# Performance work log

Measured on AMD Instinct MI355X. Metric: run time of the kernel, lower is better.

Reference implementation:

```python
import jax, jax.numpy as jnp
import numpy as np

D_MODEL = 1024
N_HEADS = 16
HEAD_DIM = D_MODEL // N_HEADS  # 64
N_T = max(1, int(N_HEADS * 0.25))  # 4 time heads
N_S = N_HEADS - N_T               # 12 space heads
T_DIM = N_T * HEAD_DIM
S_DIM = N_S * HEAD_DIM
B, L = 2, 2048


def setup_inputs() -> dict:
    key = jax.random.key(0)
    ks = jax.random.split(key, 8)
    std = 0.02
    return {
        "x": jax.random.normal(ks[0], (B, L, D_MODEL), dtype=jnp.float32),
        "attention_mask": jnp.zeros((B, 1, 1, L), dtype=jnp.float32),
        # torch nn.Linear weights have shape (out_features, in_features)
        "w_qt": jax.random.normal(ks[1], (T_DIM, D_MODEL), dtype=jnp.float32) * std,
        "w_kt": jax.random.normal(ks[2], (T_DIM, D_MODEL), dtype=jnp.float32) * std,
        "w_qs": jax.random.normal(ks[3], (S_DIM, D_MODEL), dtype=jnp.float32) * std,
        "w_ks": jax.random.normal(ks[4], (S_DIM, D_MODEL), dtype=jnp.float32) * std,
        "w_sigma": jnp.zeros((1,), dtype=jnp.float32),
        "w_v": jax.random.normal(ks[5], (D_MODEL, D_MODEL), dtype=jnp.float32) * std,
        "w_o": jax.random.normal(ks[6], (D_MODEL, D_MODEL), dtype=jnp.float32) * std,
    }


def _heads(x, w, n_h):
    # x:(B,L,D) @ w.T:(D,out) -> (B,L,n_h,d_h) -> (B,n_h,L,d_h)
    b, l, _ = x.shape
    y = jnp.einsum('bld,td->blt', x, w)
    return y.reshape(b, l, n_h, HEAD_DIM).transpose(0, 2, 1, 3)


def reference(x, attention_mask, w_qt, w_kt, w_qs, w_ks, w_sigma, w_v, w_o):
    b, l, _ = x.shape
    scale = np.sqrt(HEAD_DIM).astype(np.float32)
    # F3: time heads (sign-flipped, scaled by learnable sigma) + space heads
    Qt = _heads(x, w_qt, N_T)
    Kt = _heads(x, w_kt, N_T)
    Qs = _heads(x, w_qs, N_S)
    Ks = _heads(x, w_ks, N_S)
    st = jnp.einsum('bhqd,bhkd->bhqk', Qt, Kt)  # (B,N_T,L,L)
    ss = jnp.einsum('bhqd,bhkd->bhqk', Qs, Ks)  # (B,N_S,L,L)
    sigma = jax.nn.sigmoid(w_sigma[0])
    score = jnp.concatenate([-sigma * st, ss], axis=1) / scale  # (B,H,L,L)
    score = score + attention_mask.astype(score.dtype)
    attn_probs = jax.nn.softmax(score, axis=-1).astype(x.dtype)
    # dropout p=0.0 -> identity
    V = _heads(x, w_v, N_HEADS)  # (B,H,L,d_h)
    out = jnp.einsum('bhqk,bhkd->bhqd', attn_probs, V)
    out = out.transpose(0, 2, 1, 3).reshape(b, l, D_MODEL)
    out = jnp.einsum('bld,od->blo', out, w_o)
    return out, attn_probs
```

## Files before the change

kernel.cpp:

```cpp
#include <hip/hip_runtime.h>

typedef __bf16 bf16x8 __attribute__((ext_vector_type(8)));
typedef float f32x4 __attribute__((ext_vector_type(4)));
typedef short short4v __attribute__((ext_vector_type(4)));
typedef unsigned short ushort8 __attribute__((ext_vector_type(8)));

#define AS1 __attribute__((address_space(1)))
#define AS3 __attribute__((address_space(3)))
#define GLL16(g, l) __builtin_amdgcn_global_load_lds((const AS1 void*)(g), (AS3 void*)(l), 16, 0, 0)
#define MFMA16(a, b, c) __builtin_amdgcn_mfma_f32_16x16x32_bf16((a), (b), (c), 0, 0, 0)

__device__ __forceinline__ unsigned short f2bf(float f) {
  unsigned int u = __builtin_bit_cast(unsigned int, f);
  u = (u + 0x7fffu + ((u >> 16) & 1u)) >> 16;
  return (unsigned short)u;
}

__global__ void convert_kernel(const float* __restrict__ x,
                               const float* __restrict__ w_qt, const float* __restrict__ w_kt,
                               const float* __restrict__ w_qs, const float* __restrict__ w_ks,
                               const float* __restrict__ w_v, const float* __restrict__ w_o,
                               unsigned short* __restrict__ xb, unsigned short* __restrict__ wcat,
                               unsigned short* __restrict__ wob) {
  const int NX = 4096 * 1024, NW = 3072 * 1024, NO = 1024 * 1024;
  int stride = gridDim.x * blockDim.x;
  for (int i = blockIdx.x * blockDim.x + threadIdx.x; i < NX + NW + NO; i += stride) {
    if (i < NX) {
      xb[i] = f2bf(x[i]);
    } else if (i < NX + NW) {
      int j = i - NX;
      int n = j >> 10, k = j & 1023;
      const float* src;
      if (n < 256)        src = w_qt + n * 1024;
      else if (n < 1024)  src = w_qs + (n - 256) * 1024;
      else if (n < 1280)  src = w_kt + (n - 1024) * 1024;
      else if (n < 2048)  src = w_ks + (n - 1280) * 1024;
      else                src = w_v + (n - 2048) * 1024;
      wcat[j] = f2bf(src[k]);
    } else {
      int j = i - NX - NW;
      wob[j] = f2bf(w_o[j]);
    }
  }
}

__global__ __launch_bounds__(256) void gemm_qkv(const unsigned short* __restrict__ A,
                                                const unsigned short* __restrict__ Bw,
                                                unsigned short* __restrict__ qb,
                                                unsigned short* __restrict__ kb,
                                                unsigned short* __restrict__ vt) {
  __shared__ unsigned short As[128 * 32];
  __shared__ unsigned short Bs[128 * 32];
  const int t = threadIdx.x;
  const int lane = t & 63, wid = t >> 6;
  const int wm = wid >> 1, wn = wid & 1;
  const int lr = lane & 15, lg = lane >> 4;
  const int m0 = blockIdx.x * 128, n0 = blockIdx.y * 128;
  const int K = 1024;
  f32x4 acc[4][4] = {};
  const unsigned short* gA0 = A + (m0 + (t >> 2)) * K + (t & 3) * 8;
  const unsigned short* gB0 = Bw + (n0 + (t >> 2)) * K + (t & 3) * 8;
  char* lA = (char*)As + wid * 1024;
  char* lB = (char*)Bs + wid * 1024;
  for (int k0 = 0; k0 < K; k0 += 32) {
    __syncthreads();
    GLL16(gA0 + k0, lA);
    GLL16(gA0 + 64 * K + k0, lA + 4096);
    GLL16(gB0 + k0, lB);
    GLL16(gB0 + 64 * K + k0, lB + 4096);
    __syncthreads();
    bf16x8 af[4], bfr[4];
#pragma unroll
    for (int i = 0; i < 4; ++i) {
      af[i] = *(const bf16x8*)&As[(wm * 64 + i * 16 + lr) * 32 + lg * 8];
      bfr[i] = *(const bf16x8*)&Bs[(wn * 64 + i * 16 + lr) * 32 + lg * 8];
    }
#pragma unroll
    for (int i = 0; i < 4; ++i)
#pragma unroll
      for (int j = 0; j < 4; ++j)
        acc[i][j] = MFMA16(af[i], bfr[j], acc[i][j]);
  }
#pragma unroll
  for (int i = 0; i < 4; ++i) {
#pragma unroll
    for (int j = 0; j < 4; ++j) {
      int n = n0 + wn * 64 + j * 16 + lr;
      int mb = m0 + wm * 64 + i * 16 + lg * 4;
      f32x4 v = acc[i][j];
      if (n < 2048) {
        unsigned short* dst = (n < 1024) ? qb : kb;
        int nn = n & 1023;
        int h = nn >> 6, d = nn & 63;
#pragma unroll
        for (int r = 0; r < 4; ++r) {
          int m = mb + r;
          int b = m >> 11, l = m & 2047;
          dst[((b * 16 + h) * 2048 + l) * 64 + d] = f2bf(v[r]);
        }
      } else {
        int nn = n - 2048;
        int h = nn >> 6, d = nn & 63;
        int b = mb >> 11, l = mb & 2047;
        short4v pk;
        pk[0] = (short)f2bf(v[0]); pk[1] = (short)f2bf(v[1]);
        pk[2] = (short)f2bf(v[2]); pk[3] = (short)f2bf(v[3]);
        *(short4v*)&vt[((b * 16 + h) * 64 + d) * 2048 + l] = pk;
      }
    }
  }
}

__global__ __launch_bounds__(256, 4) void attn_kernel(const unsigned short* __restrict__ qb,
                                                      const unsigned short* __restrict__ kb,
                                                      const unsigned short* __restrict__ vt,
                                                      const float* __restrict__ mask,
                                                      const float* __restrict__ w_sigma,
                                                      float* __restrict__ probs,
                                                      unsigned short* __restrict__ ao) {
  __shared__ __align__(16) unsigned short ebuf[2][4][1280];
  __shared__ __align__(16) float pvacc[2048];
  __shared__ float psum[4][32];
  __shared__ float rinv[32];
  const int t = threadIdx.x;
  const int lane = t & 63, w = t >> 6;
  const int lr = lane & 15, lg = lane >> 4;
  const int q0 = blockIdx.x * 32;
  const int bh = blockIdx.y;
  const int b = bh >> 4, h = bh & 15;
  const float sigma = 1.0f / (1.0f + __expf(-w_sigma[0]));
  const float fac = (h < 4) ? (-sigma * 0.125f) : 0.125f;
  const float* maskb = mask + b * 2048;
  const int kbase = w * 512;

  for (int i = t; i < 2048; i += 256) pvacc[i] = 0.0f;

  bf16x8 aq[2][2];
#pragma unroll
  for (int qt = 0; qt < 2; ++qt) {
    const unsigned short* qp = qb + ((bh * 2048) + q0 + qt * 16 + lr) * 64 + lg * 8;
    aq[qt][0] = *(const bf16x8*)qp;
    aq[qt][1] = *(const bf16x8*)(qp + 32);
  }

  float rs[2][4] = {};
  for (int c = 0; c < 16; ++c) {
    int kc = kbase + c * 32;
#pragma unroll
    for (int kt = 0; kt < 2; ++kt) {
      int col = kc + kt * 16 + lr;
      const unsigned short* kp = kb + ((bh * 2048) + col) * 64 + lg * 8;
      bf16x8 b0 = *(const bf16x8*)kp;
      bf16x8 b1 = *(const bf16x8*)(kp + 32);
      float mv = maskb[col];
#pragma unroll
      for (int qt = 0; qt < 2; ++qt) {
        f32x4 acc = {};
        acc = MFMA16(aq[qt][0], b0, acc);
        acc = MFMA16(aq[qt][1], b1, acc);
#pragma unroll
        for (int r = 0; r < 4; ++r) rs[qt][r] += __expf(acc[r] * fac + mv);
      }
    }
  }
#pragma unroll
  for (int o = 1; o < 16; o <<= 1)
#pragma unroll
    for (int qt = 0; qt < 2; ++qt)
#pragma unroll
      for (int r = 0; r < 4; ++r) rs[qt][r] += __shfl_xor(rs[qt][r], o);
  if (lr == 0) {
#pragma unroll
    for (int qt = 0; qt < 2; ++qt)
#pragma unroll
      for (int r = 0; r < 4; ++r) psum[w][qt * 16 + lg * 4 + r] = rs[qt][r];
  }
  __syncthreads();
  if (t < 32) rinv[t] = 1.0f / (psum[0][t] + psum[1][t] + psum[2][t] + psum[3][t]);
  __syncthreads();

  float rv[2][4];
#pragma unroll
  for (int qt = 0; qt < 2; ++qt)
#pragma unroll
    for (int r = 0; r < 4; ++r) rv[qt][r] = rinv[qt * 16 + lg * 4 + r];

  float* pp = probs + (long long)(bh * 2048 + q0) * 2048;
  f32x4 pv[2][4] = {};
  for (int c = 0; c < 16; ++c) {
    int kc = kbase + c * 32;
    unsigned short* eb = &ebuf[c & 1][w][0];
#pragma unroll
    for (int kt = 0; kt < 2; ++kt) {
      int col = kc + kt * 16 + lr;
      const unsigned short* kp = kb + ((bh * 2048) + col) * 64 + lg * 8;
      bf16x8 b0 = *(const bf16x8*)kp;
      bf16x8 b1 = *(const bf16x8*)(kp + 32);
      float mv = maskb[col];
#pragma unroll
      for (int qt = 0; qt < 2; ++qt) {
        f32x4 acc = {};
        acc = MFMA16(aq[qt][0], b0, acc);
        acc = MFMA16(aq[qt][1], b1, acc);
#pragma unroll
        for (int r = 0; r < 4; ++r) {
          float ev = __expf(acc[r] * fac + mv);
          eb[(qt * 16 + lg * 4 + r) * 40 + kt * 16 + lr] = f2bf(ev);
          __builtin_nontemporal_store(ev * rv[qt][r],
              &pp[(qt * 16 + lg * 4 + r) * 2048 + kt * 16 + lr + kc]);
        }
      }
    }
    asm volatile("s_waitcnt lgkmcnt(0)" ::: "memory");
    bf16x8 pa[2];
#pragma unroll
    for (int qt = 0; qt < 2; ++qt)
      pa[qt] = *(const bf16x8*)&eb[(qt * 16 + lr) * 40 + lg * 8];
#pragma unroll
    for (int dt = 0; dt < 4; ++dt) {
      const unsigned short* vp = vt + ((bh * 64) + dt * 16 + lr) * 2048 + kc + lg * 8;
      bf16x8 bv = *(const bf16x8*)vp;
      pv[0][dt] = MFMA16(pa[0], bv, pv[0][dt]);
      pv[1][dt] = MFMA16(pa[1], bv, pv[1][dt]);
    }
  }

#pragma unroll
  for (int qt = 0; qt < 2; ++qt)
#pragma unroll
    for (int dt = 0; dt < 4; ++dt)
#pragma unroll
      for (int r = 0; r < 4; ++r)
        atomicAdd(&pvacc[(qt * 16 + lg * 4 + r) * 64 + dt * 16 + lr], pv[qt][dt][r]);
  __syncthreads();

  {
    int row = t >> 3, c8 = (t & 7) * 8;
    f32x4 v0 = *(const f32x4*)&pvacc[row * 64 + c8];
    f32x4 v1 = *(const f32x4*)&pvacc[row * 64 + c8 + 4];
    float ri = rinv[row];
    ushort8 o;
#pragma unroll
    for (int i = 0; i < 4; ++i) {
      o[i] = f2bf(v0[i] * ri);
      o[i + 4] = f2bf(v1[i] * ri);
    }
    *(ushort8*)&ao[((b * 2048) + q0 + row) * 1024 + h * 64 + c8] = o;
  }
}

__global__ __launch_bounds__(256) void gemm_oproj(const unsigned short* __restrict__ A,
                                                  const unsigned short* __restrict__ Bw,
                                                  float* __restrict__ out) {
  __shared__ unsigned short As[128 * 32];
  __shared__ unsigned short Bs[128 * 32];
  const int t = threadIdx.x;
  const int lane = t & 63, wid = t >> 6;
  const int wm = wid >> 1, wn = wid & 1;
  const int lr = lane & 15, lg = lane >> 4;
  const int m0 = blockIdx.x * 128, n0 = blockIdx.y * 128;
  const int K = 1024;
  f32x4 acc[4][4] = {};
  const unsigned short* gA0 = A + (m0 + (t >> 2)) * K + (t & 3) * 8;
  const unsigned short* gB0 = Bw + (n0 + (t >> 2)) * K + (t & 3) * 8;
  char* lA = (char*)As + wid * 1024;
  char* lB = (char*)Bs + wid * 1024;
  for (int k0 = 0; k0 < K; k0 += 32) {
    __syncthreads();
    GLL16(gA0 + k0, lA);
    GLL16(gA0 + 64 * K + k0, lA + 4096);
    GLL16(gB0 + k0, lB);
    GLL16(gB0 + 64 * K + k0, lB + 4096);
    __syncthreads();
    bf16x8 af[4], bfr[4];
#pragma unroll
    for (int i = 0; i < 4; ++i) {
      af[i] = *(const bf16x8*)&As[(wm * 64 + i * 16 + lr) * 32 + lg * 8];
      bfr[i] = *(const bf16x8*)&Bs[(wn * 64 + i * 16 + lr) * 32 + lg * 8];
    }
#pragma unroll
    for (int i = 0; i < 4; ++i)
#pragma unroll
      for (int j = 0; j < 4; ++j)
        acc[i][j] = MFMA16(af[i], bfr[j], acc[i][j]);
  }
#pragma unroll
  for (int i = 0; i < 4; ++i) {
#pragma unroll
    for (int j = 0; j < 4; ++j) {
      int n = n0 + wn * 64 + j * 16 + lr;
      int mb = m0 + wm * 64 + i * 16 + lg * 4;
#pragma unroll
      for (int r = 0; r < 4; ++r)
        out[(mb + r) * 1024 + n] = acc[i][j][r];
    }
  }
}

extern "C" void kernel_launch(void* const* d_in, const int* in_sizes, int n_in,
                              void* d_out, int out_size, void* d_ws, size_t ws_size,
                              hipStream_t stream) {
  const float* x       = (const float*)d_in[0];
  const float* amask   = (const float*)d_in[1];
  const float* w_qt    = (const float*)d_in[2];
  const float* w_kt    = (const float*)d_in[3];
  const float* w_qs    = (const float*)d_in[4];
  const float* w_ks    = (const float*)d_in[5];
  const float* w_sigma = (const float*)d_in[6];
  const float* w_v     = (const float*)d_in[7];
  const float* w_o     = (const float*)d_in[8];

  char* ws = (char*)d_ws;
  unsigned short* xb   = (unsigned short*)ws;
  unsigned short* wcat = (unsigned short*)(ws + 8388608);
  unsigned short* wob  = (unsigned short*)(ws + 14680064);
  unsigned short* qb   = (unsigned short*)(ws + 16777216);
  unsigned short* kb   = (unsigned short*)(ws + 25165824);
  unsigned short* vt   = (unsigned short*)(ws + 33554432);
  unsigned short* ao   = (unsigned short*)(ws + 41943040);

  float* outp = (float*)d_out;
  float* probs = outp + 4194304;

  convert_kernel<<<2048, 256, 0, stream>>>(x, w_qt, w_kt, w_qs, w_ks, w_v, w_o, xb, wcat, wob);
  gemm_qkv<<<dim3(32, 24), 256, 0, stream>>>(xb, wcat, qb, kb, vt);
  attn_kernel<<<dim3(64, 32), 256, 0, stream>>>(qb, kb, vt, amask, w_sigma, probs, ao);
  gemm_oproj<<<dim3(32, 8), 256, 0, stream>>>(ao, wob, outp);
}
```

Baseline: 340.5 us.

## Split attention into row-sum and main kernels with pre-normalized probabilities and vectorized stores

Moves the first softmax pass into a separate kernel that handles 64 query rows per block and writes the per-row negative log2 of the denominator. The main kernel then adds that term inside exp2, so probabilities come out already normalized and the final per-row rescale disappears. The probabilities are staged as fp32 in an XOR-swizzled LDS buffer, written to global memory as vectorized 16-byte nontemporal stores, and packed to bf16 with v_cvt_pk_bf16_f32 for the PV MFMA. This is meant to coalesce the large probs write and reduce exp and convert overhead, at the cost of an extra launch and a second full read of K for QK^T.

```diff
diff --git a/kernel.cpp b/kernel.cpp
--- a/kernel.cpp
+++ b/kernel.cpp
@@ -4,16 +4,24 @@
 typedef float f32x4 __attribute__((ext_vector_type(4)));
 typedef short short4v __attribute__((ext_vector_type(4)));
 typedef unsigned short ushort8 __attribute__((ext_vector_type(8)));
+typedef unsigned int uint4v __attribute__((ext_vector_type(4)));
 
 #define AS1 __attribute__((address_space(1)))
 #define AS3 __attribute__((address_space(3)))
 #define GLL16(g, l) __builtin_amdgcn_global_load_lds((const AS1 void*)(g), (AS3 void*)(l), 16, 0, 0)
 #define MFMA16(a, b, c) __builtin_amdgcn_mfma_f32_16x16x32_bf16((a), (b), (c), 0, 0, 0)
+#define L2E 1.44269504f
 
 __device__ __forceinline__ unsigned short f2bf(float f) {
   unsigned int u = __builtin_bit_cast(unsigned int, f);
   u = (u + 0x7fffu + ((u >> 16) & 1u)) >> 16;
   return (unsigned short)u;
+}
+
+__device__ __forceinline__ unsigned int cvtpk_bf16(float lo, float hi) {
+  unsigned int r;
+  asm("v_cvt_pk_bf16_f32 %0, %1, %2" : "=v"(r) : "v"(lo), "v"(hi));
+  return r;
 }
 
 __global__ void convert_kernel(const float* __restrict__ x,
@@ -111,17 +119,80 @@
   }
 }
 
-__global__ __launch_bounds__(256, 4) void attn_kernel(const unsigned short* __restrict__ qb,
+__global__ __launch_bounds__(256, 4) void attn_rowsum(const unsigned short* __restrict__ qb,
                                                       const unsigned short* __restrict__ kb,
-                                                      const unsigned short* __restrict__ vt,
                                                       const float* __restrict__ mask,
                                                       const float* __restrict__ w_sigma,
-                                                      float* __restrict__ probs,
-                                                      unsigned short* __restrict__ ao) {
-  __shared__ __align__(16) unsigned short ebuf[2][4][1280];
+                                                      float* __restrict__ rws) {
+  __shared__ float psum[4][64];
+  const int t = threadIdx.x;
+  const int lane = t & 63, w = t >> 6;
+  const int lr = lane & 15, lg = lane >> 4;
+  const int q0 = blockIdx.x * 64;
+  const int bh = blockIdx.y;
+  const int b = bh >> 4, h = bh & 15;
+  const float sigma = 1.0f / (1.0f + __expf(-w_sigma[0]));
+  const float fac2 = ((h < 4) ? (-sigma * 0.125f) : 0.125f) * L2E;
+  const float* maskb = mask + b * 2048;
+  const int kbase = w * 512;
+
+  bf16x8 aq[4][2];
+#pragma unroll
+  for (int qt = 0; qt < 4; ++qt) {
+    const unsigned short* qp = qb + ((bh * 2048) + q0 + qt * 16 + lr) * 64 + lg * 8;
+    aq[qt][0] = *(const bf16x8*)qp;
+    aq[qt][1] = *(const bf16x8*)(qp + 32);
+  }
+
+  float rs[4][4] = {};
+  for (int c = 0; c < 16; ++c) {
+    int kc = kbase + c * 32;
+#pragma unroll
+    for (int kt = 0; kt < 2; ++kt) {
+      int col = kc + kt * 16 + lr;
+      const unsigned short* kp = kb + ((bh * 2048) + col) * 64 + lg * 8;
+      bf16x8 b0 = *(const bf16x8*)kp;
+      bf16x8 b1 = *(const bf16x8*)(kp + 32);
+      float mv2 = maskb[col] * L2E;
+#pragma unroll
+      for (int qt = 0; qt < 4; ++qt) {
+        f32x4 acc = {};
+        acc = MFMA16(aq[qt][0], b0, acc);
+        acc = MFMA16(aq[qt][1], b1, acc);
+#pragma unroll
+        for (int r = 0; r < 4; ++r) rs[qt][r] += exp2f(acc[r] * fac2 + mv2);
+      }
+    }
+  }
+#pragma unroll
+  for (int o = 1; o < 16; o <<= 1)
+#pragma unroll
+    for (int qt = 0; qt < 4; ++qt)
+#pragma unroll
+      for (int r = 0; r < 4; ++r) rs[qt][r] += __shfl_xor(rs[qt][r], o);
+  if (lr == 0) {
+#pragma unroll
+    for (int qt = 0; qt < 4; ++qt)
+#pragma unroll
+      for (int r = 0; r < 4; ++r) psum[w][qt * 16 + lg * 4 + r] = rs[qt][r];
+  }
+  __syncthreads();
+  if (t < 64) {
+    float s = psum[0][t] + psum[1][t] + psum[2][t] + psum[3][t];
+    rws[bh * 2048 + q0 + t] = -log2f(s);
+  }
+}
+
+__global__ __launch_bounds__(256, 4) void attn_main(const unsigned short* __restrict__ qb,
+                                                    const unsigned short* __restrict__ kb,
+                                                    const unsigned short* __restrict__ vt,
+                                                    const float* __restrict__ mask,
+                                                    const float* __restrict__ w_sigma,
+                                                    const float* __restrict__ rws,
+                                                    float* __restrict__ probs,
+                                                    unsigned short* __restrict__ ao) {
+  __shared__ __align__(16) char ebuf[4][4096];
   __shared__ __align__(16) float pvacc[2048];
-  __shared__ float psum[4][32];
-  __shared__ float rinv[32];
   const int t = threadIdx.x;
   const int lane = t & 63, w = t >> 6;
   const int lr = lane & 15, lg = lane >> 4;
@@ -129,21 +200,28 @@
   const int bh = blockIdx.y;
   const int b = bh >> 4, h = bh & 15;
   const float sigma = 1.0f / (1.0f + __expf(-w_sigma[0]));
-  const float fac = (h < 4) ? (-sigma * 0.125f) : 0.125f;
+  const float fac2 = ((h < 4) ? (-sigma * 0.125f) : 0.125f) * L2E;
   const float* maskb = mask + b * 2048;
   const int kbase = w * 512;
 
   for (int i = t; i < 2048; i += 256) pvacc[i] = 0.0f;
+  __syncthreads();
 
   bf16x8 aq[2][2];
+  float lr2[2][4];
 #pragma unroll
   for (int qt = 0; qt < 2; ++qt) {
     const unsigned short* qp = qb + ((bh * 2048) + q0 + qt * 16 + lr) * 64 + lg * 8;
     aq[qt][0] = *(const bf16x8*)qp;
     aq[qt][1] = *(const bf16x8*)(qp + 32);
-  }
-
-  float rs[2][4] = {};
+#pragma unroll
+    for (int r = 0; r < 4; ++r)
+      lr2[qt][r] = rws[bh * 2048 + q0 + qt * 16 + lg * 4 + r];
+  }
+
+  char* eb = ebuf[w];
+  float* pp = probs + (long long)(bh * 2048 + q0) * 2048;
+  f32x4 pv[2][4] = {};
   for (int c = 0; c < 16; ++c) {
     int kc = kbase + c * 32;
 #pragma unroll
@@ -152,70 +230,40 @@
       const unsigned short* kp = kb + ((bh * 2048) + col) * 64 + lg * 8;
       bf16x8 b0 = *(const bf16x8*)kp;
       bf16x8 b1 = *(const bf16x8*)(kp + 32);
-      float mv = maskb[col];
+      float mv2 = maskb[col] * L2E;
 #pragma unroll
       for (int qt = 0; qt < 2; ++qt) {
         f32x4 acc = {};
         acc = MFMA16(aq[qt][0], b0, acc);
         acc = MFMA16(aq[qt][1], b1, acc);
 #pragma unroll
-        for (int r = 0; r < 4; ++r) rs[qt][r] += __expf(acc[r] * fac + mv);
-      }
-    }
-  }
-#pragma unroll
-  for (int o = 1; o < 16; o <<= 1)
-#pragma unroll
-    for (int qt = 0; qt < 2; ++qt)
-#pragma unroll
-      for (int r = 0; r < 4; ++r) rs[qt][r] += __shfl_xor(rs[qt][r], o);
-  if (lr == 0) {
-#pragma unroll
-    for (int qt = 0; qt < 2; ++qt)
-#pragma unroll
-      for (int r = 0; r < 4; ++r) psum[w][qt * 16 + lg * 4 + r] = rs[qt][r];
-  }
-  __syncthreads();
-  if (t < 32) rinv[t] = 1.0f / (psum[0][t] + psum[1][t] + psum[2][t] + psum[3][t]);
-  __syncthreads();
-
-  float rv[2][4];
-#pragma unroll
-  for (int qt = 0; qt < 2; ++qt)
-#pragma unroll
-    for (int r = 0; r < 4; ++r) rv[qt][r] = rinv[qt * 16 + lg * 4 + r];
-
-  float* pp = probs + (long long)(bh * 2048 + q0) * 2048;
-  f32x4 pv[2][4] = {};
-  for (int c = 0; c < 16; ++c) {
-    int kc = kbase + c * 32;
-    unsigned short* eb = &ebuf[c & 1][w][0];
-#pragma unroll
-    for (int kt = 0; kt < 2; ++kt) {
-      int col = kc + kt * 16 + lr;
-      const unsigned short* kp = kb + ((bh * 2048) + col) * 64 + lg * 8;
-      bf16x8 b0 = *(const bf16x8*)kp;
-      bf16x8 b1 = *(const bf16x8*)(kp + 32);
-      float mv = maskb[col];
-#pragma unroll
-      for (int qt = 0; qt < 2; ++qt) {
-        f32x4 acc = {};
-        acc = MFMA16(aq[qt][0], b0, acc);
-        acc = MFMA16(aq[qt][1], b1, acc);
-#pragma unroll
         for (int r = 0; r < 4; ++r) {
-          float ev = __expf(acc[r] * fac + mv);
-          eb[(qt * 16 + lg * 4 + r) * 40 + kt * 16 + lr] = f2bf(ev);
-          __builtin_nontemporal_store(ev * rv[qt][r],
-              &pp[(qt * 16 + lg * 4 + r) * 2048 + kt * 16 + lr + kc]);
+          int row = qt * 16 + lg * 4 + r;
+          float p = exp2f(acc[r] * fac2 + mv2 + lr2[qt][r]);
+          int off = (row * 128 + (kt * 16 + lr) * 4) ^ ((row & 7) << 4);
+          *(float*)(eb + off) = p;
         }
       }
     }
     asm volatile("s_waitcnt lgkmcnt(0)" ::: "memory");
     bf16x8 pa[2];
 #pragma unroll
-    for (int qt = 0; qt < 2; ++qt)
-      pa[qt] = *(const bf16x8*)&eb[(qt * 16 + lr) * 40 + lg * 8];
+    for (int qt = 0; qt < 2; ++qt) {
+      int row = qt * 16 + lr;
+      int base = row * 128 + lg * 32;
+      int sw = (row & 7) << 4;
+      f32x4 v0 = *(const f32x4*)(eb + (base ^ sw));
+      f32x4 v1 = *(const f32x4*)(eb + ((base + 16) ^ sw));
+      float* dst = pp + row * 2048 + kc + lg * 8;
+      __builtin_nontemporal_store(v0, (f32x4*)dst);
+      __builtin_nontemporal_store(v1, (f32x4*)(dst + 4));
+      uint4v u;
+      u[0] = cvtpk_bf16(v0[0], v0[1]);
+      u[1] = cvtpk_bf16(v0[2], v0[3]);
+      u[2] = cvtpk_bf16(v1[0], v1[1]);
+      u[3] = cvtpk_bf16(v1[2], v1[3]);
+      pa[qt] = __builtin_bit_cast(bf16x8, u);
+    }
 #pragma unroll
     for (int dt = 0; dt < 4; ++dt) {
       const unsigned short* vp = vt + ((bh * 64) + dt * 16 + lr) * 2048 + kc + lg * 8;
@@ -238,12 +286,11 @@
     int row = t >> 3, c8 = (t & 7) * 8;
     f32x4 v0 = *(const f32x4*)&pvacc[row * 64 + c8];
     f32x4 v1 = *(const f32x4*)&pvacc[row * 64 + c8 + 4];
-    float ri = rinv[row];
     ushort8 o;
 #pragma unroll
     for (int i = 0; i < 4; ++i) {
-      o[i] = f2bf(v0[i] * ri);
-      o[i + 4] = f2bf(v1[i] * ri);
+      o[i] = f2bf(v0[i]);
+      o[i + 4] = f2bf(v1[i]);
     }
     *(ushort8*)&ao[((b * 2048) + q0 + row) * 1024 + h * 64 + c8] = o;
   }
@@ -318,12 +365,14 @@
   unsigned short* kb   = (unsigned short*)(ws + 25165824);
   unsigned short* vt   = (unsigned short*)(ws + 33554432);
   unsigned short* ao   = (unsigned short*)(ws + 41943040);
+  float* rws           = (float*)(ws + 50331648);
 
   float* outp = (float*)d_out;
   float* probs = outp + 4194304;
 
   convert_kernel<<<2048, 256, 0, stream>>>(x, w_qt, w_kt, w_qs, w_ks, w_v, w_o, xb, wcat, wob);
   gemm_qkv<<<dim3(32, 24), 256, 0, stream>>>(xb, wcat, qb, kb, vt);
-  attn_kernel<<<dim3(64, 32), 256, 0, stream>>>(qb, kb, vt, amask, w_sigma, probs, ao);
+  attn_rowsum<<<dim3(32, 32), 256, 0, stream>>>(qb, kb, amask, w_sigma, rws);
+  attn_main<<<dim3(64, 32), 256, 0, stream>>>(qb, kb, vt, amask, w_sigma, rws, probs, ao);
   gemm_oproj<<<dim3(32, 8), 256, 0, stream>>>(ao, wob, outp);
 }
```

After: 404.9 us. 18.9% more time.

## Switch attention kernel to 32x32 MFMA tiles with exp2 and folded normalization

Applied to the files above, without the earlier changes.

Rewrites the attention kernel to use 32x32x16 bf16 MFMA instructions instead of 16x16x32, so each wave computes a 32x32 score tile and 32x64 PV outputs. Softmax uses exp2 with log2e pre-scaling, and the row normalization is folded into the exponent as minus log2 of the row sum. Probabilities are therefore already normalized before the PV product, and the final per-row rescale goes away. The P tile is staged in a swizzled LDS layout to avoid bank conflicts, and launch bounds drop to 3 blocks per CU because register use is higher.

```diff
diff --git a/kernel.cpp b/kernel.cpp
--- a/kernel.cpp
+++ b/kernel.cpp
@@ -2,6 +2,7 @@
 
 typedef __bf16 bf16x8 __attribute__((ext_vector_type(8)));
 typedef float f32x4 __attribute__((ext_vector_type(4)));
+typedef float f32x16 __attribute__((ext_vector_type(16)));
 typedef short short4v __attribute__((ext_vector_type(4)));
 typedef unsigned short ushort8 __attribute__((ext_vector_type(8)));
 
@@ -9,6 +10,8 @@
 #define AS3 __attribute__((address_space(3)))
 #define GLL16(g, l) __builtin_amdgcn_global_load_lds((const AS1 void*)(g), (AS3 void*)(l), 16, 0, 0)
 #define MFMA16(a, b, c) __builtin_amdgcn_mfma_f32_16x16x32_bf16((a), (b), (c), 0, 0, 0)
+#define MFMA32(a, b, c) __builtin_amdgcn_mfma_f32_32x32x16_bf16((a), (b), (c), 0, 0, 0)
+#define L2E 1.44269504f
 
 __device__ __forceinline__ unsigned short f2bf(float f) {
   unsigned int u = __builtin_bit_cast(unsigned int, f);
@@ -111,139 +114,123 @@
   }
 }
 
-__global__ __launch_bounds__(256, 4) void attn_kernel(const unsigned short* __restrict__ qb,
+__global__ __launch_bounds__(256, 3) void attn_kernel(const unsigned short* __restrict__ qb,
                                                       const unsigned short* __restrict__ kb,
                                                       const unsigned short* __restrict__ vt,
                                                       const float* __restrict__ mask,
                                                       const float* __restrict__ w_sigma,
                                                       float* __restrict__ probs,
                                                       unsigned short* __restrict__ ao) {
-  __shared__ __align__(16) unsigned short ebuf[2][4][1280];
+  __shared__ __align__(16) char plds[4][2048];
   __shared__ __align__(16) float pvacc[2048];
   __shared__ float psum[4][32];
-  __shared__ float rinv[32];
+  __shared__ float rsum[32];
   const int t = threadIdx.x;
   const int lane = t & 63, w = t >> 6;
-  const int lr = lane & 15, lg = lane >> 4;
+  const int col = lane & 31;
+  const int hi = lane >> 5;
+  const int koff = hi * 8;
   const int q0 = blockIdx.x * 32;
   const int bh = blockIdx.y;
   const int b = bh >> 4, h = bh & 15;
   const float sigma = 1.0f / (1.0f + __expf(-w_sigma[0]));
-  const float fac = (h < 4) ? (-sigma * 0.125f) : 0.125f;
+  const float fac2 = ((h < 4) ? (-sigma * 0.125f) : 0.125f) * L2E;
   const float* maskb = mask + b * 2048;
   const int kbase = w * 512;
 
   for (int i = t; i < 2048; i += 256) pvacc[i] = 0.0f;
 
-  bf16x8 aq[2][2];
-#pragma unroll
-  for (int qt = 0; qt < 2; ++qt) {
-    const unsigned short* qp = qb + ((bh * 2048) + q0 + qt * 16 + lr) * 64 + lg * 8;
-    aq[qt][0] = *(const bf16x8*)qp;
-    aq[qt][1] = *(const bf16x8*)(qp + 32);
-  }
-
-  float rs[2][4] = {};
+  bf16x8 qf[4];
+  const unsigned short* qp = qb + (size_t)(bh * 2048 + q0 + col) * 64 + koff;
+#pragma unroll
+  for (int m = 0; m < 4; ++m) qf[m] = *(const bf16x8*)(qp + m * 16);
+
+  float rs[16];
+#pragma unroll
+  for (int r = 0; r < 16; ++r) rs[r] = 0.0f;
   for (int c = 0; c < 16; ++c) {
     int kc = kbase + c * 32;
-#pragma unroll
-    for (int kt = 0; kt < 2; ++kt) {
-      int col = kc + kt * 16 + lr;
-      const unsigned short* kp = kb + ((bh * 2048) + col) * 64 + lg * 8;
-      bf16x8 b0 = *(const bf16x8*)kp;
-      bf16x8 b1 = *(const bf16x8*)(kp + 32);
-      float mv = maskb[col];
-#pragma unroll
-      for (int qt = 0; qt < 2; ++qt) {
-        f32x4 acc = {};
-        acc = MFMA16(aq[qt][0], b0, acc);
-        acc = MFMA16(aq[qt][1], b1, acc);
-#pragma unroll
-        for (int r = 0; r < 4; ++r) rs[qt][r] += __expf(acc[r] * fac + mv);
-      }
-    }
-  }
-#pragma unroll
-  for (int o = 1; o < 16; o <<= 1)
-#pragma unroll
-    for (int qt = 0; qt < 2; ++qt)
-#pragma unroll
-      for (int r = 0; r < 4; ++r) rs[qt][r] += __shfl_xor(rs[qt][r], o);
-  if (lr == 0) {
-#pragma unroll
-    for (int qt = 0; qt < 2; ++qt)
-#pragma unroll
-      for (int r = 0; r < 4; ++r) psum[w][qt * 16 + lg * 4 + r] = rs[qt][r];
+    const unsigned short* kp = kb + (size_t)(bh * 2048 + kc + col) * 64 + koff;
+    f32x16 s = {};
+#pragma unroll
+    for (int m = 0; m < 4; ++m) s = MFMA32(qf[m], *(const bf16x8*)(kp + m * 16), s);
+    float mv2 = maskb[kc + col] * L2E;
+#pragma unroll
+    for (int r = 0; r < 16; ++r) rs[r] += exp2f(s[r] * fac2 + mv2);
+  }
+#pragma unroll
+  for (int o = 1; o < 32; o <<= 1)
+#pragma unroll
+    for (int r = 0; r < 16; ++r) rs[r] += __shfl_xor(rs[r], o);
+  if (col == 0) {
+#pragma unroll
+    for (int r = 0; r < 16; ++r) psum[w][(r & 3) + 8 * (r >> 2) + 4 * hi] = rs[r];
   }
   __syncthreads();
-  if (t < 32) rinv[t] = 1.0f / (psum[0][t] + psum[1][t] + psum[2][t] + psum[3][t]);
+  if (t < 32) rsum[t] = -log2f(psum[0][t] + psum[1][t] + psum[2][t] + psum[3][t]);
   __syncthreads();
 
-  float rv[2][4];
-#pragma unroll
-  for (int qt = 0; qt < 2; ++qt)
-#pragma unroll
-    for (int r = 0; r < 4; ++r) rv[qt][r] = rinv[qt * 16 + lg * 4 + r];
-
-  float* pp = probs + (long long)(bh * 2048 + q0) * 2048;
-  f32x4 pv[2][4] = {};
+  float rws_l[16];
+#pragma unroll
+  for (int r = 0; r < 16; ++r) rws_l[r] = rsum[(r & 3) + 8 * (r >> 2) + 4 * hi];
+
+  char* pl = plds[w];
+  float* pp = probs + (size_t)(bh * 2048 + q0) * 2048;
+  f32x16 oacc[2] = {};
   for (int c = 0; c < 16; ++c) {
     int kc = kbase + c * 32;
-    unsigned short* eb = &ebuf[c & 1][w][0];
-#pragma unroll
-    for (int kt = 0; kt < 2; ++kt) {
-      int col = kc + kt * 16 + lr;
-      const unsigned short* kp = kb + ((bh * 2048) + col) * 64 + lg * 8;
-      bf16x8 b0 = *(const bf16x8*)kp;
-      bf16x8 b1 = *(const bf16x8*)(kp + 32);
-      float mv = maskb[col];
-#pragma unroll
-      for (int qt = 0; qt < 2; ++qt) {
-        f32x4 acc = {};
-        acc = MFMA16(aq[qt][0], b0, acc);
-        acc = MFMA16(aq[qt][1], b1, acc);
-#pragma unroll
-        for (int r = 0; r < 4; ++r) {
-          float ev = __expf(acc[r] * fac + mv);
-          eb[(qt * 16 + lg * 4 + r) * 40 + kt * 16 + lr] = f2bf(ev);
-          __builtin_nontemporal_store(ev * rv[qt][r],
-              &pp[(qt * 16 + lg * 4 + r) * 2048 + kt * 16 + lr + kc]);
-        }
+    const unsigned short* kp = kb + (size_t)(bh * 2048 + kc + col) * 64 + koff;
+    f32x16 s = {};
+#pragma unroll
+    for (int m = 0; m < 4; ++m) s = MFMA32(qf[m], *(const bf16x8*)(kp + m * 16), s);
+    float mv2 = maskb[kc + col] * L2E;
+    float p[16];
+#pragma unroll
+    for (int r = 0; r < 16; ++r) p[r] = exp2f(s[r] * fac2 + (rws_l[r] + mv2));
+    float* pr = pp + kc + col;
+#pragma unroll
+    for (int r = 0; r < 16; ++r) {
+      int row = (r & 3) + 8 * (r >> 2) + 4 * hi;
+      __builtin_nontemporal_store(p[r], pr + row * 2048);
+    }
+#pragma unroll
+    for (int r = 0; r < 16; ++r) {
+      int row = (r & 3) + 8 * (r >> 2) + 4 * hi;
+      int off = (row * 64 + col * 2) ^ ((row & 7) << 4);
+      *(unsigned short*)(pl + off) = f2bf(p[r]);
+    }
+    asm volatile("" ::: "memory");
+#pragma unroll
+    for (int kh = 0; kh < 2; ++kh) {
+      int arow = col;
+      int aoff = (arow * 64 + (kh * 16 + koff) * 2) ^ ((arow & 7) << 4);
+      bf16x8 pa = *(const bf16x8*)(pl + aoff);
+#pragma unroll
+      for (int dh = 0; dh < 2; ++dh) {
+        const unsigned short* vp = vt + (size_t)(bh * 64 + dh * 32 + col) * 2048 + kc + kh * 16 + koff;
+        oacc[dh] = MFMA32(pa, *(const bf16x8*)vp, oacc[dh]);
       }
     }
-    asm volatile("s_waitcnt lgkmcnt(0)" ::: "memory");
-    bf16x8 pa[2];
-#pragma unroll
-    for (int qt = 0; qt < 2; ++qt)
-      pa[qt] = *(const bf16x8*)&eb[(qt * 16 + lr) * 40 + lg * 8];
-#pragma unroll
-    for (int dt = 0; dt < 4; ++dt) {
-      const unsigned short* vp = vt + ((bh * 64) + dt * 16 + lr) * 2048 + kc + lg * 8;
-      bf16x8 bv = *(const bf16x8*)vp;
-      pv[0][dt] = MFMA16(pa[0], bv, pv[0][dt]);
-      pv[1][dt] = MFMA16(pa[1], bv, pv[1][dt]);
-    }
-  }
-
-#pragma unroll
-  for (int qt = 0; qt < 2; ++qt)
-#pragma unroll
-    for (int dt = 0; dt < 4; ++dt)
-#pragma unroll
-      for (int r = 0; r < 4; ++r)
-        atomicAdd(&pvacc[(qt * 16 + lg * 4 + r) * 64 + dt * 16 + lr], pv[qt][dt][r]);
+  }
+
+#pragma unroll
+  for (int dh = 0; dh < 2; ++dh)
+#pragma unroll
+    for (int r = 0; r < 16; ++r) {
+      int row = (r & 3) + 8 * (r >> 2) + 4 * hi;
+      atomicAdd(&pvacc[row * 64 + dh * 32 + col], oacc[dh][r]);
+    }
   __syncthreads();
 
   {
     int row = t >> 3, c8 = (t & 7) * 8;
     f32x4 v0 = *(const f32x4*)&pvacc[row * 64 + c8];
     f32x4 v1 = *(const f32x4*)&pvacc[row * 64 + c8 + 4];
-    float ri = rinv[row];
     ushort8 o;
 #pragma unroll
     for (int i = 0; i < 4; ++i) {
-      o[i] = f2bf(v0[i] * ri);
-      o[i + 4] = f2bf(v1[i] * ri);
+      o[i] = f2bf(v0[i]);
+      o[i + 4] = f2bf(v1[i]);
     }
     *(ushort8*)&ao[((b * 2048) + q0 + row) * 1024 + h * 64 + c8] = o;
   }
```

Measured after the change: 348.5 us. 2.3% more time.
